# Optimization experiments

Hardware: AMD Instinct MI355X
Metric: run time of the kernel (lower is better)

## Reference

```python
import jax, jax.numpy as jnp
import numpy as np

B, S, H = 2, 4096, 2048
NH, HD = 16, 128
BLOCK = 256
EPS = 1e-5


def setup_inputs() -> dict:
    key = jax.random.key(0)
    ks = jax.random.split(key, 6)
    return {
        "hidden_states": jax.random.normal(ks[0], (B, S, H), jnp.float32),
        "attention_mask": jnp.ones((B, S), jnp.float32),
        "slope_rate": jax.random.uniform(ks[1], (NH,), jnp.float32),
        "w_qkv": jax.random.normal(ks[2], (H, 3 * NH * HD), jnp.float32) * 0.02,
        "w_gate": jax.random.normal(ks[3], (H, NH * HD), jnp.float32) * 0.02,
        "w_out": jax.random.normal(ks[4], (NH * HD, H), jnp.float32) * 0.02,
        "norm_weight": jnp.ones((NH * HD,), jnp.float32),
    }


def _lightning_attention(q, k, v, slope):
    # q,k,v: [b,h,n,d]; slope: [h] positive decay rates
    b, h, n, d = q.shape
    nc = n // BLOCK
    ar = jnp.arange(BLOCK, dtype=q.dtype) + 1.0  # 1..BLOCK
    s = slope[:, None, None]  # [h,1,1]
    q_decay = jnp.exp(-s * ar[None, :, None])             # [h,BLOCK,1]
    k_decay = jnp.exp(-s * (BLOCK - ar)[None, :, None])   # [h,BLOCK,1]
    idx = ar[:, None] - ar[None, :]                        # [BLOCK,BLOCK]
    mask = (idx >= 0).astype(q.dtype)
    # mask idx before exp so masked entries don't overflow (keeps grads finite)
    diag_decay = jnp.exp(-s * (idx * mask)[None]) * mask[None]  # [h,BLOCK,BLOCK]
    block_decay = jnp.exp(-slope * BLOCK)[None, :, None, None]  # [1,h,1,1]

    def to_chunks(x):
        return x.reshape(b, h, nc, BLOCK, d).transpose(2, 0, 1, 3, 4)

    qc, kc, vc = to_chunks(q), to_chunks(k), to_chunks(v)

    def step(kv, xs):
        qi, ki, vi = xs  # [b,h,BLOCK,d]
        # inter-chunk: decayed query against carried state kv [b,h,d,d]
        o_inter = jnp.einsum("bhmd,bhde->bhme", qi * q_decay, kv)
        # intra-chunk: causal decayed attention
        attn = jnp.einsum("bhmd,bhnd->bhmn", qi, ki) * diag_decay
        o = o_inter + jnp.einsum("bhmn,bhne->bhme", attn, vi)
        kv = block_decay * kv + jnp.einsum("bhnd,bhne->bhde", ki * k_decay, vi)
        return kv, o

    kv0 = jnp.zeros((b, h, d, d), q.dtype)
    _, o = jax.lax.scan(step, kv0, (qc, kc, vc))  # o: [nc,b,h,BLOCK,d]
    return o.transpose(1, 2, 0, 3, 4).reshape(b, h, n, d)


def reference(hidden_states, attention_mask, slope_rate, w_qkv, w_gate, w_out, norm_weight):
    b, n, _ = hidden_states.shape
    qkv = jax.nn.silu(hidden_states @ w_qkv)  # act on fused qkv
    q, k, v = jnp.split(qkv, 3, axis=-1)

    def heads(x):
        return x.reshape(b, n, NH, HD).transpose(0, 2, 1, 3)

    q, k, v = heads(q), heads(k), heads(v)
    v = v * attention_mask[:, None, :, None]  # zero padded tokens
    o = _lightning_attention(q, k, v, slope_rate)  # [b,h,n,d]
    o = o.transpose(0, 2, 1, 3).reshape(b, n, NH * HD)
    # RMSNorm over head_dim*num_heads
    var = jnp.mean(o * o, axis=-1, keepdims=True)
    o = o * jax.lax.rsqrt(var + EPS) * norm_weight
    # sigmoid output gate from raw hidden_states
    o = jax.nn.sigmoid(hidden_states @ w_gate) * o
    return o @ w_out
```

## Files before the change

kernel.cpp:

```cpp
#include <hip/hip_runtime.h>
#include <cstdint>

#define B_ 2
#define S_ 4096
#define H_ 2048
#define NH_ 16
#define HD_ 128
#define BLOCK_ 256
#define NC_ (S_/BLOCK_)
#define M_ (B_*S_)
#define EPS_ 1e-5f

typedef unsigned short ushort_t;
typedef unsigned short u16x4 __attribute__((ext_vector_type(4)));
typedef short frag_ab __attribute__((ext_vector_type(8)));
typedef float frag_cd __attribute__((ext_vector_type(4)));

static __device__ inline float bf2f(ushort_t u) {
    union { unsigned int i; float f; } x;
    x.i = ((unsigned int)u) << 16;
    return x.f;
}
static __device__ inline ushort_t f2bf(float f) {
    union { float f; unsigned int i; } x;
    x.f = f;
    unsigned int r = x.i + 0x7fffu + ((x.i >> 16) & 1u);
    return (ushort_t)(r >> 16);
}

static __device__ __forceinline__ void gload_lds16(const ushort_t* g, ushort_t* l) {
    __builtin_amdgcn_global_load_lds(
        (__attribute__((address_space(1))) void*)(uintptr_t)g,
        (__attribute__((address_space(3))) void*)l,
        16, 0, 0);
}

#define FENCE_ asm volatile("" ::: "memory")
#define VMW8_  asm volatile("s_waitcnt vmcnt(8)" ::: "memory")
#define VMW2_  asm volatile("s_waitcnt vmcnt(2)" ::: "memory")
#define VMW0_  asm volatile("s_waitcnt vmcnt(0)" ::: "memory")

__global__ __launch_bounds__(256)
void cast_bf16_kernel(const float* __restrict__ in, ushort_t* __restrict__ out)
{
    int i = blockIdx.x * 256 + threadIdx.x;
    float4 v = reinterpret_cast<const float4*>(in)[i];
    u16x4 o = { f2bf(v.x), f2bf(v.y), f2bf(v.z), f2bf(v.w) };
    *reinterpret_cast<u16x4*>(&out[(size_t)i * 4]) = o;
}

__global__ __launch_bounds__(256)
void transpose_cast_kernel(const float* __restrict__ W, ushort_t* __restrict__ WT,
                           int K, int N)
{
    __shared__ float t[32][33];
    const int kb = blockIdx.y * 32, nb = blockIdx.x * 32;
    const int tx = threadIdx.x & 31, ty = threadIdx.x >> 5;
    #pragma unroll
    for (int i = 0; i < 4; ++i)
        t[ty + i * 8][tx] = W[(size_t)(kb + ty + i * 8) * N + nb + tx];
    __syncthreads();
    #pragma unroll
    for (int i = 0; i < 4; ++i)
        WT[(size_t)(nb + ty + i * 8) * K + kb + tx] = f2bf(t[tx][ty + i * 8]);
}

template<int MODE>
__global__ __launch_bounds__(512, 2)
void gemm256(const ushort_t* __restrict__ A, const ushort_t* __restrict__ BT,
             int M, int N, int K,
             float* __restrict__ Cf,
             ushort_t* __restrict__ qo, ushort_t* __restrict__ ko,
             ushort_t* __restrict__ kTo, ushort_t* __restrict__ vTo,
             ushort_t* __restrict__ gateo, const float* __restrict__ mask)
{
    __shared__ __align__(16) ushort_t LA[2][16384];
    __shared__ __align__(16) ushort_t LB[2][16384];

    const int tid  = threadIdx.x;
    const int lane = tid & 63, wid = tid >> 6;
    const int wm = wid >> 2, wn = wid & 3;
    const int l15 = lane & 15, l4 = lane >> 4;
    const int trow = tid >> 3;
    const int xk   = (tid & 7) ^ (trow & 7);

    const int nwg = gridDim.x;
    const int lin = blockIdx.x;
    const int virt = (lin & 7) * (nwg >> 3) + (lin >> 3);
    const int NBX = N >> 8;
    const int by = virt / NBX, bx = virt - by * NBX;
    const int rowBase = by * 256, colBase = bx * 256;

    frag_cd acc[8][4];
    #pragma unroll
    for (int m = 0; m < 8; ++m)
        #pragma unroll
        for (int n = 0; n < 4; ++n) acc[m][n] = 0.f;

    frag_ab fa[4][2];
    frag_ab fb[2][2][2];

    #define RDF(Lp, row_, sl_) \
        (*reinterpret_cast<const frag_ab*>( \
            reinterpret_cast<const char*>(Lp) + (row_) * 128 + ((((sl_) ^ ((row_) & 7)) & 7) << 4)))
    #define STG(Gp, base_, i_, kt_, Lp) \
        gload_lds16((Gp) + (size_t)((base_) + (i_) * 64 + trow) * K + (kt_) + xk * 8, \
                    (Lp) + (i_) * 4096 + wid * 512)

    const int NT = K >> 6;
    int cur = 0;
    STG(BT, colBase, 0, 0, LB[0]); STG(BT, colBase, 1, 0, LB[0]);
    STG(BT, colBase, 2, 0, LB[0]); STG(BT, colBase, 3, 0, LB[0]);
    STG(A,  rowBase, 0, 0, LA[0]); STG(A,  rowBase, 2, 0, LA[0]);
    STG(A,  rowBase, 1, 0, LA[0]); STG(A,  rowBase, 3, 0, LA[0]);
    VMW2_; FENCE_; __builtin_amdgcn_s_barrier();
    __builtin_amdgcn_sched_barrier(0);

    for (int t = 0; t < NT; ++t) {
        const ushort_t* Ab = LA[cur];
        const ushort_t* Bb = LB[cur];
        ushort_t* An = LA[cur ^ 1];
        ushort_t* Bn = LB[cur ^ 1];
        const int ktn = (t + 1) << 6;
        const bool more = (t + 1) < NT;

        #pragma unroll
        for (int mi = 0; mi < 4; ++mi)
            #pragma unroll
            for (int ks = 0; ks < 2; ++ks)
                fa[mi][ks] = RDF(Ab, wm * 128 + mi * 16 + l15, ks * 4 + l4);
        #pragma unroll
        for (int ni = 0; ni < 2; ++ni)
            #pragma unroll
            for (int ks = 0; ks < 2; ++ks)
                fb[0][ni][ks] = RDF(Bb, wn * 64 + ni * 16 + l15, ks * 4 + l4);
        if (more) {
            STG(BT, colBase, 0, ktn, Bn); STG(BT, colBase, 1, ktn, Bn);
            STG(BT, colBase, 2, ktn, Bn); STG(BT, colBase, 3, ktn, Bn);
            STG(A,  rowBase, 0, ktn, An); STG(A,  rowBase, 2, ktn, An);
        }
        __builtin_amdgcn_s_setprio(1);
        #pragma unroll
        for (int mi = 0; mi < 4; ++mi)
            #pragma unroll
            for (int ni = 0; ni < 2; ++ni)
                #pragma unroll
                for (int ks = 0; ks < 2; ++ks)
                    acc[mi][ni] = __builtin_amdgcn_mfma_f32_16x16x32_bf16(
                        fa[mi][ks], fb[0][ni][ks], acc[mi][ni], 0, 0, 0);
        __builtin_amdgcn_s_setprio(0);

        #pragma unroll
        for (int ni = 0; ni < 2; ++ni)
            #pragma unroll
            for (int ks = 0; ks < 2; ++ks)
                fb[1][ni][ks] = RDF(Bb, wn * 64 + 32 + ni * 16 + l15, ks * 4 + l4);
        if (more) { STG(A, rowBase, 1, ktn, An); STG(A, rowBase, 3, ktn, An); }
        __builtin_amdgcn_s_setprio(1);
        #pragma unroll
        for (int mi = 0; mi < 4; ++mi)
            #pragma unroll
            for (int ni = 0; ni < 2; ++ni)
                #pragma unroll
                for (int ks = 0; ks < 2; ++ks)
                    acc[mi][2 + ni] = __builtin_amdgcn_mfma_f32_16x16x32_bf16(
                        fa[mi][ks], fb[1][ni][ks], acc[mi][2 + ni], 0, 0, 0);
        __builtin_amdgcn_s_setprio(0);
        if (more) { VMW8_; } else { VMW0_; }
        FENCE_; __builtin_amdgcn_s_barrier();
        __builtin_amdgcn_sched_barrier(0);

        #pragma unroll
        for (int mi = 0; mi < 4; ++mi)
            #pragma unroll
            for (int ks = 0; ks < 2; ++ks)
                fa[mi][ks] = RDF(Ab, wm * 128 + 64 + mi * 16 + l15, ks * 4 + l4);
        __builtin_amdgcn_s_setprio(1);
        #pragma unroll
        for (int mi = 0; mi < 4; ++mi)
            #pragma unroll
            for (int ni = 0; ni < 2; ++ni)
                #pragma unroll
                for (int ks = 0; ks < 2; ++ks)
                    acc[4 + mi][ni] = __builtin_amdgcn_mfma_f32_16x16x32_bf16(
                        fa[mi][ks], fb[0][ni][ks], acc[4 + mi][ni], 0, 0, 0);
        __builtin_amdgcn_s_setprio(0);

        __builtin_amdgcn_s_setprio(1);
        #pragma unroll
        for (int mi = 0; mi < 4; ++mi)
            #pragma unroll
            for (int ni = 0; ni < 2; ++ni)
                #pragma unroll
                for (int ks = 0; ks < 2; ++ks)
                    acc[4 + mi][2 + ni] = __builtin_amdgcn_mfma_f32_16x16x32_bf16(
                        fa[mi][ks], fb[1][ni][ks], acc[4 + mi][2 + ni], 0, 0, 0);
        __builtin_amdgcn_s_setprio(0);
        if (more) { VMW2_; }
        FENCE_; __builtin_amdgcn_s_barrier();
        __builtin_amdgcn_sched_barrier(0);

        cur ^= 1;
    }
    #undef RDF
    #undef STG

    const int row0 = rowBase + wm * 128;
    const int c0   = colBase + wn * 64;
    if (MODE == 0) {
        #pragma unroll
        for (int m = 0; m < 8; ++m) {
            int mr = (m >> 2) * 64 + (m & 3) * 16;
            #pragma unroll
            for (int n = 0; n < 4; ++n) {
                int nc = (n >> 1) * 32 + (n & 1) * 16;
                #pragma unroll
                for (int r = 0; r < 4; ++r) {
                    int row = row0 + mr + l4 * 4 + r;
                    int col = c0 + nc + l15;
                    Cf[(size_t)row * N + col] = acc[m][n][r];
                }
            }
        }
    } else {
        const int which = c0 >> 11;
        const int h     = (c0 >> 7) & 15;
        const int d0    = c0 & 127;
        const int b     = row0 >> 12;
        const int bh    = b * NH_ + h;
        #pragma unroll
        for (int m = 0; m < 8; ++m) {
            int mr = (m >> 2) * 64 + (m & 3) * 16;
            int sr0 = (row0 & 4095) + mr + l4 * 4;
            #pragma unroll
            for (int n = 0; n < 4; ++n) {
                int nc = (n >> 1) * 32 + (n & 1) * 16;
                float x0 = acc[m][n][0], x1 = acc[m][n][1];
                float x2 = acc[m][n][2], x3 = acc[m][n][3];
                if (which == 3) {
                    int col_g = (c0 - 6144) + nc + l15;
                    ushort_t* gp = gateo + (size_t)(row0 + mr + l4 * 4) * H_ + col_g;
                    gp[0]       = f2bf(1.f / (1.f + __expf(-x0)));
                    gp[H_]      = f2bf(1.f / (1.f + __expf(-x1)));
                    gp[2 * H_]  = f2bf(1.f / (1.f + __expf(-x2)));
                    gp[3 * H_]  = f2bf(1.f / (1.f + __expf(-x3)));
                } else {
                    int d = d0 + nc + l15;
                    float s0 = x0 / (1.f + __expf(-x0));
                    float s1 = x1 / (1.f + __expf(-x1));
                    float s2 = x2 / (1.f + __expf(-x2));
                    float s3 = x3 / (1.f + __expf(-x3));
                    if (which == 0) {
                        ushort_t* qp = qo + ((size_t)bh * S_ + sr0) * HD_ + d;
                        qp[0]        = f2bf(s0);
                        qp[HD_]      = f2bf(s1);
                        qp[2 * HD_]  = f2bf(s2);
                        qp[3 * HD_]  = f2bf(s3);
                    } else if (which == 1) {
                        u16x4 pk = { f2bf(s0), f2bf(s1), f2bf(s2), f2bf(s3) };
                        ushort_t* kp = ko + ((size_t)bh * S_ + sr0) * HD_ + d;
                        kp[0] = pk[0]; kp[HD_] = pk[1]; kp[2 * HD_] = pk[2]; kp[3 * HD_] = pk[3];
                        *reinterpret_cast<u16x4*>(&kTo[((size_t)bh * HD_ + d) * S_ + sr0]) = pk;
                    } else {
                        float mk0 = mask[b * S_ + sr0],     mk1 = mask[b * S_ + sr0 + 1];
                        float mk2 = mask[b * S_ + sr0 + 2], mk3 = mask[b * S_ + sr0 + 3];
                        u16x4 pk = { f2bf(s0 * mk0), f2bf(s1 * mk1), f2bf(s2 * mk2), f2bf(s3 * mk3) };
                        *reinterpret_cast<u16x4*>(&vTo[((size_t)bh * HD_ + d) * S_ + sr0]) = pk;
                    }
                }
            }
        }
    }
}

__global__ __launch_bounds__(256)
void kv_chunk_mfma(const ushort_t* __restrict__ kT, const ushort_t* __restrict__ vT,
                   const float* __restrict__ slope, ushort_t* __restrict__ kvT)
{
    const int c = blockIdx.x, bh = blockIdx.y;
    const float s = slope[bh & 15];
    const int tid = threadIdx.x, lane = tid & 63, w = tid >> 6;
    const int l15 = lane & 15, l4 = lane >> 4;
    __shared__ float dec[BLOCK_];
    __shared__ __align__(16) ushort_t VTl[128 * 64];
    __shared__ __align__(16) ushort_t KTl[128 * 64];
    dec[tid] = __expf(-s * (float)(BLOCK_ - 1 - tid));

    frag_cd acc[2][8];
    #pragma unroll
    for (int mf = 0; mf < 2; ++mf)
        #pragma unroll
        for (int df = 0; df < 8; ++df) acc[mf][df] = 0.f;

    for (int nt = 0; nt < 4; ++nt) {
        __syncthreads();
        #pragma unroll
        for (int i = 0; i < 4; ++i) {
            int u = tid + i * 256;
            int row = u >> 3, slot = u & 7;
            size_t gsrc = ((size_t)bh * HD_ + row) * S_ + c * BLOCK_ + nt * 64 + slot * 8;
            frag_ab v8 = *reinterpret_cast<const frag_ab*>(vT + gsrc);
            *reinterpret_cast<frag_ab*>((char*)VTl + row * 128 + ((slot * 16) ^ ((row & 7) << 4))) = v8;
            frag_ab k8 = *reinterpret_cast<const frag_ab*>(kT + gsrc);
            frag_ab kd;
            #pragma unroll
            for (int j = 0; j < 8; ++j)
                kd[j] = (short)f2bf(bf2f((ushort_t)k8[j]) * dec[nt * 64 + slot * 8 + j]);
            *reinterpret_cast<frag_ab*>((char*)KTl + row * 128 + ((slot * 16) ^ ((row & 7) << 4))) = kd;
        }
        __syncthreads();
        #pragma unroll
        for (int ks = 0; ks < 2; ++ks) {
            frag_ab a[2];
            #pragma unroll
            for (int mf = 0; mf < 2; ++mf)
                a[mf] = *reinterpret_cast<const frag_ab*>(
                    (char*)VTl + (w * 32 + mf * 16 + l15) * 128 + ((ks * 64 + l4 * 16) ^ ((l15 & 7) << 4)));
            #pragma unroll
            for (int df = 0; df < 8; ++df) {
                frag_ab bk = *reinterpret_cast<const frag_ab*>(
                    (char*)KTl + (df * 16 + l15) * 128 + ((ks * 64 + l4 * 16) ^ ((l15 & 7) << 4)));
                acc[0][df] = __builtin_amdgcn_mfma_f32_16x16x32_bf16(a[0], bk, acc[0][df], 0, 0, 0);
                acc[1][df] = __builtin_amdgcn_mfma_f32_16x16x32_bf16(a[1], bk, acc[1][df], 0, 0, 0);
            }
        }
    }
    ushort_t* out = kvT + ((size_t)bh * NC_ + c) * 16384;
    #pragma unroll
    for (int mf = 0; mf < 2; ++mf)
        #pragma unroll
        for (int df = 0; df < 8; ++df)
            #pragma unroll
            for (int r = 0; r < 4; ++r) {
                int e = w * 32 + mf * 16 + l4 * 4 + r;
                int d = df * 16 + l15;
                out[e * 128 + d] = f2bf(acc[mf][df][r]);
            }
}

__global__ __launch_bounds__(256)
void kv_scan_kernel(const float* __restrict__ slope, const ushort_t* __restrict__ kvT,
                    ushort_t* __restrict__ sT)
{
    const int es = blockIdx.x, bh = blockIdx.y;
    const float s = slope[bh & 15];
    const float bd = __expf(-s * (float)BLOCK_);
    const int tid = threadIdx.x;
    float st[16];
    #pragma unroll
    for (int i = 0; i < 16; ++i) st[i] = 0.f;
    for (int c = 0; c < NC_; ++c) {
        const ushort_t* p = kvT + ((size_t)bh * NC_ + c) * 16384;
        ushort_t* qp = sT + ((size_t)bh * NC_ + c) * 16384;
        #pragma unroll
        for (int i = 0; i < 16; ++i) {
            int lin = tid + i * 256;
            int off = (lin >> 5) * 128 + es * 32 + (lin & 31);
            float x = bf2f(p[off]);
            qp[off] = f2bf(st[i]);
            st[i] = bd * st[i] + x;
        }
    }
}

__global__ __launch_bounds__(512)
void attn_mfma(const ushort_t* __restrict__ q, const ushort_t* __restrict__ k,
               const ushort_t* __restrict__ vT, const ushort_t* __restrict__ sT,
               const float* __restrict__ slope, float* __restrict__ o)
{
    const int c = blockIdx.x, bh = blockIdx.y;
    const int h = bh & 15, b = bh >> 4;
    const float s = slope[h];
    const int tid = threadIdx.x, lane = tid & 63, w = tid >> 6;
    const int l15 = lane & 15, l4 = lane >> 4;

    __shared__ __align__(16) ushort_t SH[16384];
    __shared__ __align__(16) ushort_t P[8][2048];

    frag_ab aq[2][4];
    #pragma unroll
    for (int mf = 0; mf < 2; ++mf)
        #pragma unroll
        for (int ks = 0; ks < 4; ++ks) {
            int row = c * BLOCK_ + w * 32 + mf * 16 + l15;
            aq[mf][ks] = *reinterpret_cast<const frag_ab*>(
                q + ((size_t)bh * S_ + row) * HD_ + ks * 32 + l4 * 8);
        }

    frag_cd oa[2][8];
    #pragma unroll
    for (int mf = 0; mf < 2; ++mf)
        #pragma unroll
        for (int ef = 0; ef < 8; ++ef) oa[mf][ef] = 0.f;

    const int wrow = w * 32;
    for (int nt = 0; nt < 4; ++nt) {
        __syncthreads();
        #pragma unroll
        for (int i = 0; i < 2; ++i) {
            int u = tid + i * 512;
            int n = u >> 4, slot = u & 15;
            frag_ab k8 = *reinterpret_cast<const frag_ab*>(
                k + ((size_t)bh * S_ + c * BLOCK_ + nt * 64 + n) * HD_ + slot * 8);
            *reinterpret_cast<frag_ab*>((char*)SH + n * 256 + ((slot * 16) ^ ((n & 7) << 4))) = k8;
        }
        #pragma unroll
        for (int i = 0; i < 2; ++i) {
            int u = tid + i * 512;
            int e = u >> 3, slot = u & 7;
            frag_ab v8 = *reinterpret_cast<const frag_ab*>(
                vT + ((size_t)bh * HD_ + e) * S_ + c * BLOCK_ + nt * 64 + slot * 8);
            *reinterpret_cast<frag_ab*>((char*)SH + 16384 + e * 128 + ((slot * 16) ^ ((e & 7) << 4))) = v8;
        }
        __syncthreads();
        if (nt * 64 > wrow + 31) continue;

        frag_cd pacc[2][4];
        #pragma unroll
        for (int mf = 0; mf < 2; ++mf)
            #pragma unroll
            for (int nf = 0; nf < 4; ++nf) pacc[mf][nf] = 0.f;
        #pragma unroll
        for (int ks = 0; ks < 4; ++ks)
            #pragma unroll
            for (int nf = 0; nf < 4; ++nf) {
                frag_ab bk = *reinterpret_cast<const frag_ab*>(
                    (char*)SH + (nf * 16 + l15) * 256 + ((ks * 64 + l4 * 16) ^ ((l15 & 7) << 4)));
                pacc[0][nf] = __builtin_amdgcn_mfma_f32_16x16x32_bf16(aq[0][ks], bk, pacc[0][nf], 0, 0, 0);
                pacc[1][nf] = __builtin_amdgcn_mfma_f32_16x16x32_bf16(aq[1][ks], bk, pacc[1][nf], 0, 0, 0);
            }
        #pragma unroll
        for (int mf = 0; mf < 2; ++mf)
            #pragma unroll
            for (int nf = 0; nf < 4; ++nf)
                #pragma unroll
                for (int r = 0; r < 4; ++r) {
                    int m = mf * 16 + l4 * 4 + r;
                    int mrow = wrow + m;
                    int ncol = nt * 64 + nf * 16 + l15;
                    float pv = 0.f;
                    if (mrow >= ncol) pv = pacc[mf][nf][r] * __expf(s * (float)(ncol - mrow));
                    *reinterpret_cast<ushort_t*>(
                        (char*)&P[w][0] + m * 128 + (((nf * 16 + l15) * 2) ^ ((m & 7) << 4))) = f2bf(pv);
                }
        __builtin_amdgcn_sched_barrier(0);
        #pragma unroll
        for (int ks = 0; ks < 2; ++ks) {
            frag_ab ap[2];
            #pragma unroll
            for (int mf = 0; mf < 2; ++mf)
                ap[mf] = *reinterpret_cast<const frag_ab*>(
                    (char*)&P[w][0] + (mf * 16 + l15) * 128 + ((ks * 64 + l4 * 16) ^ ((l15 & 7) << 4)));
            #pragma unroll
            for (int ef = 0; ef < 8; ++ef) {
                frag_ab bv = *reinterpret_cast<const frag_ab*>(
                    (char*)SH + 16384 + (ef * 16 + l15) * 128 + ((ks * 64 + l4 * 16) ^ ((l15 & 7) << 4)));
                oa[0][ef] = __builtin_amdgcn_mfma_f32_16x16x32_bf16(ap[0], bv, oa[0][ef], 0, 0, 0);
                oa[1][ef] = __builtin_amdgcn_mfma_f32_16x16x32_bf16(ap[1], bv, oa[1][ef], 0, 0, 0);
            }
        }
    }

    __syncthreads();
    #pragma unroll
    for (int i = 0; i < 4; ++i) {
        int u = tid + i * 512;
        int e = u >> 4, slot = u & 15;
        frag_ab s8 = *reinterpret_cast<const frag_ab*>(
            sT + ((size_t)(bh * NC_ + c)) * 16384 + e * 128 + slot * 8);
        *reinterpret_cast<frag_ab*>((char*)SH + e * 256 + ((slot * 16) ^ ((e & 7) << 4))) = s8;
    }
    __syncthreads();
    #pragma unroll
    for (int mf = 0; mf < 2; ++mf) {
        float qd = __expf(-s * (float)(wrow + mf * 16 + l15 + 1));
        #pragma unroll
        for (int ks = 0; ks < 4; ++ks) {
            frag_ab v = aq[mf][ks];
            #pragma unroll
            for (int j = 0; j < 8; ++j)
                v[j] = (short)f2bf(bf2f((ushort_t)v[j]) * qd);
            aq[mf][ks] = v;
        }
    }
    #pragma unroll
    for (int ks = 0; ks < 4; ++ks)
        #pragma unroll
        for (int ef = 0; ef < 8; ++ef) {
            frag_ab bs = *reinterpret_cast<const frag_ab*>(
                (char*)SH + (ef * 16 + l15) * 256 + ((ks * 64 + l4 * 16) ^ ((l15 & 7) << 4)));
            oa[0][ef] = __builtin_amdgcn_mfma_f32_16x16x32_bf16(aq[0][ks], bs, oa[0][ef], 0, 0, 0);
            oa[1][ef] = __builtin_amdgcn_mfma_f32_16x16x32_bf16(aq[1][ks], bs, oa[1][ef], 0, 0, 0);
        }
    #pragma unroll
    for (int mf = 0; mf < 2; ++mf)
        #pragma unroll
        for (int ef = 0; ef < 8; ++ef)
            #pragma unroll
            for (int r = 0; r < 4; ++r) {
                int row = c * BLOCK_ + wrow + mf * 16 + l4 * 4 + r;
                int col = h * HD_ + ef * 16 + l15;
                o[((size_t)(b * S_ + row)) * H_ + col] = oa[mf][ef][r];
            }
}

__global__ __launch_bounds__(256)
void norm_gate_kernel(const float* __restrict__ o, const ushort_t* __restrict__ gate,
                      const float* __restrict__ nw, ushort_t* __restrict__ on)
{
    const int row = blockIdx.x;
    const int tid = threadIdx.x;
    const float* orow = o + (size_t)row * H_;
    const ushort_t* grow = gate + (size_t)row * H_;
    ushort_t* onrow = on + (size_t)row * H_;
    float vals[8];
    float ss = 0.f;
    #pragma unroll
    for (int i = 0; i < 8; ++i) {
        vals[i] = orow[tid + i * 256];
        ss += vals[i] * vals[i];
    }
    __shared__ float red[256];
    red[tid] = ss;
    __syncthreads();
    #pragma unroll
    for (int st = 128; st > 0; st >>= 1) {
        if (tid < st) red[tid] += red[tid + st];
        __syncthreads();
    }
    float scale = rsqrtf(red[0] * (1.f / (float)H_) + EPS_);
    #pragma unroll
    for (int i = 0; i < 8; ++i) {
        int cidx = tid + i * 256;
        onrow[cidx] = f2bf(vals[i] * scale * nw[cidx] * bf2f(grow[cidx]));
    }
}

extern "C" void kernel_launch(void* const* d_in, const int* in_sizes, int n_in,
                              void* d_out, int out_size, void* d_ws, size_t ws_size,
                              hipStream_t stream)
{
    const float* hidden = (const float*)d_in[0];
    const float* mask   = (const float*)d_in[1];
    const float* slope  = (const float*)d_in[2];
    const float* w_qkv  = (const float*)d_in[3];
    const float* w_gate = (const float*)d_in[4];
    const float* w_out  = (const float*)d_in[5];
    const float* nw     = (const float*)d_in[6];

    const size_t MH = (size_t)M_ * H_;
    ushort_t* hid_bf  = (ushort_t*)d_ws;
    ushort_t* on_ws   = hid_bf;
    ushort_t* wqkvT   = hid_bf + MH;
    ushort_t* wgateT  = wqkvT + (size_t)6144 * 2048;
    ushort_t* kvT_ws  = wqkvT;
    ushort_t* sT_ws   = wqkvT + MH / 2;
    ushort_t* woutT   = wqkvT;
    ushort_t* q_ws    = hid_bf + 2 * MH;
    ushort_t* k_ws    = q_ws + MH;
    ushort_t* vT_ws   = k_ws + MH;
    ushort_t* gate_ws = vT_ws + MH;
    ushort_t* kT_ws   = (ushort_t*)d_out;
    float*    o_f32   = (float*)d_out;

    dim3 blk(256);
    cast_bf16_kernel<<<(MH / 4) / 256, blk, 0, stream>>>(hidden, hid_bf);
    transpose_cast_kernel<<<dim3(6144 / 32, 2048 / 32), blk, 0, stream>>>(w_qkv, wqkvT, 2048, 6144);
    transpose_cast_kernel<<<dim3(2048 / 32, 2048 / 32), blk, 0, stream>>>(w_gate, wgateT, 2048, 2048);
    gemm256<2><<<dim3((M_ / 256) * (8192 / 256)), dim3(512), 0, stream>>>(
        hid_bf, wqkvT, M_, 8192, 2048,
        nullptr, q_ws, k_ws, kT_ws, vT_ws, gate_ws, mask);
    kv_chunk_mfma<<<dim3(NC_, B_ * NH_), blk, 0, stream>>>(kT_ws, vT_ws, slope, kvT_ws);
    kv_scan_kernel<<<dim3(4, B_ * NH_), blk, 0, stream>>>(slope, kvT_ws, sT_ws);
    attn_mfma<<<dim3(NC_, B_ * NH_), dim3(512), 0, stream>>>(
        q_ws, k_ws, vT_ws, sT_ws, slope, o_f32);
    transpose_cast_kernel<<<dim3(2048 / 32, 2048 / 32), blk, 0, stream>>>(w_out, woutT, 2048, 2048);
    norm_gate_kernel<<<M_, blk, 0, stream>>>(o_f32, gate_ws, nw, on_ws);
    gemm256<0><<<dim3((M_ / 256) * (2048 / 256)), dim3(512), 0, stream>>>(
        on_ws, woutT, M_, 2048, 2048,
        (float*)d_out, nullptr, nullptr, nullptr, nullptr, nullptr, nullptr);
}
```

Before: 566.0 us.

## Use 128x128 GEMM for output projection and rebalance global-load staging in gemm256

Replaces the 256x256-tile GEMM used for the output projection (M=8192, N=2048) with a new 128x128-tile, 256-thread kernel. The new kernel launches 1024 workgroups instead of 256, which should fill the GPU's compute units more evenly. It also spreads the prefetch global-to-LDS loads more evenly across the four MFMA phases of the gemm256 main loop, so memory issue overlaps better with the matrix instructions. The smaller tiles give less data reuse per workgroup, and the simpler single-phase pipeline may hide latency less well. The MODE 0 epilogue is removed from gemm256.

New measurement: 559.1 us. Within noise of the previous version (-1.2%).

```diff
diff --git a/kernel.cpp b/kernel.cpp
--- a/kernel.cpp
+++ b/kernel.cpp
@@ -134,11 +134,7 @@
             #pragma unroll
             for (int ks = 0; ks < 2; ++ks)
                 fb[0][ni][ks] = RDF(Bb, wn * 64 + ni * 16 + l15, ks * 4 + l4);
-        if (more) {
-            STG(BT, colBase, 0, ktn, Bn); STG(BT, colBase, 1, ktn, Bn);
-            STG(BT, colBase, 2, ktn, Bn); STG(BT, colBase, 3, ktn, Bn);
-            STG(A,  rowBase, 0, ktn, An); STG(A,  rowBase, 2, ktn, An);
-        }
+        if (more) { STG(BT, colBase, 0, ktn, Bn); STG(BT, colBase, 1, ktn, Bn); }
         __builtin_amdgcn_s_setprio(1);
         #pragma unroll
         for (int mi = 0; mi < 4; ++mi)
@@ -155,7 +151,7 @@
             #pragma unroll
             for (int ks = 0; ks < 2; ++ks)
                 fb[1][ni][ks] = RDF(Bb, wn * 64 + 32 + ni * 16 + l15, ks * 4 + l4);
-        if (more) { STG(A, rowBase, 1, ktn, An); STG(A, rowBase, 3, ktn, An); }
+        if (more) { STG(BT, colBase, 2, ktn, Bn); STG(BT, colBase, 3, ktn, Bn); }
         __builtin_amdgcn_s_setprio(1);
         #pragma unroll
         for (int mi = 0; mi < 4; ++mi)
@@ -175,6 +171,7 @@
             #pragma unroll
             for (int ks = 0; ks < 2; ++ks)
                 fa[mi][ks] = RDF(Ab, wm * 128 + 64 + mi * 16 + l15, ks * 4 + l4);
+        if (more) { STG(A, rowBase, 0, ktn, An); STG(A, rowBase, 2, ktn, An); }
         __builtin_amdgcn_s_setprio(1);
         #pragma unroll
         for (int mi = 0; mi < 4; ++mi)
@@ -186,6 +183,7 @@
                         fa[mi][ks], fb[0][ni][ks], acc[4 + mi][ni], 0, 0, 0);
         __builtin_amdgcn_s_setprio(0);
 
+        if (more) { STG(A, rowBase, 1, ktn, An); STG(A, rowBase, 3, ktn, An); }
         __builtin_amdgcn_s_setprio(1);
         #pragma unroll
         for (int mi = 0; mi < 4; ++mi)
@@ -207,22 +205,7 @@
 
     const int row0 = rowBase + wm * 128;
     const int c0   = colBase + wn * 64;
-    if (MODE == 0) {
-        #pragma unroll
-        for (int m = 0; m < 8; ++m) {
-            int mr = (m >> 2) * 64 + (m & 3) * 16;
-            #pragma unroll
-            for (int n = 0; n < 4; ++n) {
-                int nc = (n >> 1) * 32 + (n & 1) * 16;
-                #pragma unroll
-                for (int r = 0; r < 4; ++r) {
-                    int row = row0 + mr + l4 * 4 + r;
-                    int col = c0 + nc + l15;
-                    Cf[(size_t)row * N + col] = acc[m][n][r];
-                }
-            }
-        }
-    } else {
+    {
         const int which = c0 >> 11;
         const int h     = (c0 >> 7) & 15;
         const int d0    = c0 & 127;
@@ -273,6 +256,106 @@
     }
 }
 
+__global__ __launch_bounds__(256, 2)
+void gemm128(const ushort_t* __restrict__ A, const ushort_t* __restrict__ BT,
+             int M, int N, int K, float* __restrict__ Cf)
+{
+    __shared__ __align__(16) ushort_t LA[2][8192];
+    __shared__ __align__(16) ushort_t LB[2][8192];
+
+    const int tid  = threadIdx.x;
+    const int lane = tid & 63, wid = tid >> 6;
+    const int wm = wid >> 1, wn = wid & 1;
+    const int l15 = lane & 15, l4 = lane >> 4;
+    const int trow = tid >> 3;
+    const int xk   = (tid & 7) ^ (trow & 7);
+
+    const int nwg = gridDim.x;
+    const int lin = blockIdx.x;
+    const int virt = (lin & 7) * (nwg >> 3) + (lin >> 3);
+    const int NBX = N >> 7;
+    const int by = virt / NBX, bx = virt - by * NBX;
+    const int rowBase = by * 128, colBase = bx * 128;
+
+    frag_cd acc[4][4];
+    #pragma unroll
+    for (int m = 0; m < 4; ++m)
+        #pragma unroll
+        for (int n = 0; n < 4; ++n) acc[m][n] = 0.f;
+
+    frag_ab fa[4][2];
+    frag_ab fb[4][2];
+
+    #define RDF(Lp, row_, sl_) \
+        (*reinterpret_cast<const frag_ab*>( \
+            reinterpret_cast<const char*>(Lp) + (row_) * 128 + ((((sl_) ^ ((row_) & 7)) & 7) << 4)))
+    #define STG(Gp, base_, i_, kt_, Lp) \
+        gload_lds16((Gp) + (size_t)((base_) + (i_) * 32 + trow) * K + (kt_) + xk * 8, \
+                    (Lp) + (i_) * 2048 + wid * 512)
+
+    const int NT = K >> 6;
+    int cur = 0;
+    #pragma unroll
+    for (int i = 0; i < 4; ++i) { STG(A, rowBase, i, 0, LA[0]); STG(BT, colBase, i, 0, LB[0]); }
+    VMW0_; FENCE_; __builtin_amdgcn_s_barrier();
+    __builtin_amdgcn_sched_barrier(0);
+
+    for (int t = 0; t < NT; ++t) {
+        const ushort_t* Ab = LA[cur];
+        const ushort_t* Bb = LB[cur];
+        ushort_t* An = LA[cur ^ 1];
+        ushort_t* Bn = LB[cur ^ 1];
+        const int ktn = (t + 1) << 6;
+        const bool more = (t + 1) < NT;
+
+        if (more) {
+            #pragma unroll
+            for (int i = 0; i < 4; ++i) { STG(A, rowBase, i, ktn, An); STG(BT, colBase, i, ktn, Bn); }
+        }
+
+        #pragma unroll
+        for (int ni = 0; ni < 4; ++ni)
+            #pragma unroll
+            for (int ks = 0; ks < 2; ++ks)
+                fb[ni][ks] = RDF(Bb, wn * 64 + ni * 16 + l15, ks * 4 + l4);
+        #pragma unroll
+        for (int mi = 0; mi < 4; ++mi)
+            #pragma unroll
+            for (int ks = 0; ks < 2; ++ks)
+                fa[mi][ks] = RDF(Ab, wm * 64 + mi * 16 + l15, ks * 4 + l4);
+
+        __builtin_amdgcn_s_setprio(1);
+        #pragma unroll
+        for (int mi = 0; mi < 4; ++mi)
+            #pragma unroll
+            for (int ni = 0; ni < 4; ++ni)
+                #pragma unroll
+                for (int ks = 0; ks < 2; ++ks)
+                    acc[mi][ni] = __builtin_amdgcn_mfma_f32_16x16x32_bf16(
+                        fa[mi][ks], fb[ni][ks], acc[mi][ni], 0, 0, 0);
+        __builtin_amdgcn_s_setprio(0);
+
+        VMW0_; FENCE_; __builtin_amdgcn_s_barrier();
+        __builtin_amdgcn_sched_barrier(0);
+        cur ^= 1;
+    }
+    #undef RDF
+    #undef STG
+
+    const int row0 = rowBase + wm * 64;
+    const int c0   = colBase + wn * 64;
+    #pragma unroll
+    for (int m = 0; m < 4; ++m)
+        #pragma unroll
+        for (int n = 0; n < 4; ++n)
+            #pragma unroll
+            for (int r = 0; r < 4; ++r) {
+                int row = row0 + m * 16 + l4 * 4 + r;
+                int col = c0 + n * 16 + l15;
+                Cf[(size_t)row * N + col] = acc[m][n][r];
+            }
+}
+
 __global__ __launch_bounds__(256)
 void kv_chunk_mfma(const ushort_t* __restrict__ kT, const ushort_t* __restrict__ vT,
                    const float* __restrict__ slope, ushort_t* __restrict__ kvT)
@@ -576,7 +659,6 @@
         q_ws, k_ws, vT_ws, sT_ws, slope, o_f32);
     transpose_cast_kernel<<<dim3(2048 / 32, 2048 / 32), blk, 0, stream>>>(w_out, woutT, 2048, 2048);
     norm_gate_kernel<<<M_, blk, 0, stream>>>(o_f32, gate_ws, nw, on_ws);
-    gemm256<0><<<dim3((M_ / 256) * (2048 / 256)), dim3(512), 0, stream>>>(
-        on_ws, woutT, M_, 2048, 2048,
-        (float*)d_out, nullptr, nullptr, nullptr, nullptr, nullptr, nullptr);
-}
+    gemm128<<<dim3((M_ / 128) * (2048 / 128)), blk, 0, stream>>>(
+        on_ws, woutT, M_, 2048, 2048, (float*)d_out);
+}
```
